# Optimization experiments

Measured on AMD Instinct MI355X. Metric: run time of the kernel, lower is better.

The kernel has to match this reference:

```python
import jax, jax.numpy as jnp
import numpy as np

KS = [3, 3, 7, 7, 11, 11, 21, 21]  # TEXT_KERNEL_SIZES
KMAX = 21
H = 8
D_MODEL = 1024
D_H = D_MODEL // H
R = 4
B = 2
N = 4096


def _extract_windows_1d(xh, k):
    # xh: (B, n, d_h) -> windows: (B, n, k, d_h), zero-padded, stride 1
    pad = k // 2
    xp = jnp.pad(xh, ((0, 0), (pad, pad), (0, 0)))
    idx = jnp.arange(xh.shape[1])[:, None] + jnp.arange(k)[None, :]  # (n, k)
    return xp[:, idx]  # (B, n, k, d_h)


def setup_inputs() -> dict:
    key = jax.random.key(0)
    ks = jax.random.split(key, 10)
    s = 0.02
    return {
        "x": jax.random.normal(ks[0], (B, N, D_MODEL), dtype=jnp.float32),
        "W_in": jax.random.normal(ks[1], (D_MODEL, D_MODEL), dtype=jnp.float32) * s,
        "b_in": jnp.zeros((D_MODEL,), dtype=jnp.float32),
        "W_out": jax.random.normal(ks[2], (D_MODEL, D_MODEL), dtype=jnp.float32) * (0.02 / np.sqrt(2.0 * 8)),
        "b_out": jnp.zeros((D_MODEL,), dtype=jnp.float32),
        "Wc": jax.random.normal(ks[3], (H, D_H, R), dtype=jnp.float32) * s,  # per-token coeff proj
        "A": jax.random.normal(ks[4], (H, R, KMAX), dtype=jnp.float32) * s,  # rank -> kernel-pos factor (padded to KMAX)
        "V": jax.random.normal(ks[5], (H, R, D_H), dtype=jnp.float32) * s,   # rank -> channel factor
        "base": jax.random.normal(ks[6], (H, KMAX, D_H), dtype=jnp.float32) * s,  # static kernel (padded)
        "alphas": jnp.zeros((H,), dtype=jnp.float32),  # sigmoid gate params
    }


def reference(x, W_in, b_in, W_out, b_out, Wc, A, V, base, alphas):
    Bsz, n, d = x.shape
    x_proj = x @ W_in.T + b_in                        # (B, n, d_model)
    x_heads = x_proj.reshape(Bsz, n, H, D_H)          # (B, n, H, d_h)
    head_outs = []
    for h in range(H):
        k = KS[h]
        x_h = x_heads[:, :, h, :]                     # (B, n, d_h)
        # Factored per-token kernel generation
        c = x_h @ Wc[h]                               # (B, n, R)
        dyn = jnp.einsum('bnr,rk,rd->bnkd', c, A[h, :, :k], V[h])  # (B, n, k, d_h)
        alpha = jax.nn.sigmoid(alphas[h])
        K_hat = alpha * dyn + (1.0 - alpha) * base[h, :k][None, None]  # (B, n, k, d_h)
        windows = _extract_windows_1d(x_h, k)         # (B, n, k, d_h)
        o_h = jnp.einsum('bnkd,bnkd->bnd', K_hat, windows)
        head_outs.append(o_h)
    concat = jnp.concatenate(head_outs, axis=-1)      # (B, n, d_model)
    return concat @ W_out.T + b_out
```

## Files before the change

### kernel.cpp

```cpp
#include <hip/hip_runtime.h>
#include <stdint.h>

typedef __bf16 bf16;
typedef __bf16 bf16x8 __attribute__((ext_vector_type(8)));
typedef float f32x4 __attribute__((ext_vector_type(4)));

#define AS1 __attribute__((address_space(1)))
#define AS3 __attribute__((address_space(3)))

__device__ __forceinline__ void gload_lds16(const void* g, void* l) {
    __builtin_amdgcn_global_load_lds((const AS1 uint32_t*)g, (AS3 uint32_t*)l, 16, 0, 0);
}

#define BM 128
#define BN 128
#define BK 32

__global__ __launch_bounds__(256, 2) void gemm_nt(
    const bf16* __restrict__ A, const bf16* __restrict__ B,
    const float* __restrict__ bias, float* __restrict__ C,
    int M, int N, int K)
{
    __shared__ bf16 smA[BM * BK];
    __shared__ bf16 smB[BN * BK];

    const int tid  = threadIdx.x;
    const int wave = tid >> 6;
    const int lane = tid & 63;
    const int wm = (wave >> 1) * 64;
    const int wn = (wave & 1) * 64;
    const int rowA0 = blockIdx.x * BM;
    const int rowB0 = blockIdx.y * BN;

    f32x4 acc[4][4] = {};

    const int g  = lane >> 4;
    const int rm = lane & 15;

    for (int k0 = 0; k0 < K; k0 += BK) {
        #pragma unroll
        for (int i = 0; i < 2; ++i) {
            int slot = i * 256 + tid;
            int row  = slot >> 2;
            int kgs  = slot & 3;
            int kd   = kgs ^ ((row >> 1) & 3);
            const bf16* ga = A + (size_t)(rowA0 + row) * K + k0 + kd * 8;
            const bf16* gb = B + (size_t)(rowB0 + row) * K + k0 + kd * 8;
            int ldsbase = (i * 256 + (wave << 6)) * 8;
            gload_lds16(ga, &smA[ldsbase]);
            gload_lds16(gb, &smB[ldsbase]);
        }
        __syncthreads();

        bf16x8 af[4], bfr[4];
        #pragma unroll
        for (int mi = 0; mi < 4; ++mi) {
            int row  = wm + mi * 16 + rm;
            int slot = row * 4 + (g ^ ((row >> 1) & 3));
            af[mi] = *(const bf16x8*)&smA[slot * 8];
        }
        #pragma unroll
        for (int ni = 0; ni < 4; ++ni) {
            int row  = wn + ni * 16 + rm;
            int slot = row * 4 + (g ^ ((row >> 1) & 3));
            bfr[ni] = *(const bf16x8*)&smB[slot * 8];
        }
        #pragma unroll
        for (int mi = 0; mi < 4; ++mi)
            #pragma unroll
            for (int ni = 0; ni < 4; ++ni)
                acc[mi][ni] = __builtin_amdgcn_mfma_f32_16x16x32_bf16(
                    af[mi], bfr[ni], acc[mi][ni], 0, 0, 0);
        __syncthreads();
    }

    const int quad = lane >> 4;
    #pragma unroll
    for (int ni = 0; ni < 4; ++ni) {
        int col = rowB0 + wn + ni * 16 + rm;
        float bcol = bias[col];
        #pragma unroll
        for (int mi = 0; mi < 4; ++mi) {
            #pragma unroll
            for (int r = 0; r < 4; ++r) {
                int rowc = rowA0 + wm + mi * 16 + quad * 4 + r;
                C[(size_t)rowc * N + col] = acc[mi][ni][r] + bcol;
            }
        }
    }
}

__global__ void cast_all_kernel(const float* __restrict__ x, bf16* __restrict__ xb,
                                const float* __restrict__ wi, bf16* __restrict__ wib,
                                const float* __restrict__ wo, bf16* __restrict__ wob)
{
    const int NX8 = (2 * 4096 * 1024) / 8;
    const int NW8 = (1024 * 1024) / 8;
    int i = blockIdx.x * 256 + threadIdx.x;
    const float* in; bf16* out; int idx;
    if (i < NX8)            { in = x;  out = xb;  idx = i; }
    else if (i < NX8 + NW8) { in = wi; out = wib; idx = i - NX8; }
    else                    { in = wo; out = wob; idx = i - NX8 - NW8; }
    const float4* p = (const float4*)in;
    float4 a = p[2 * idx], b = p[2 * idx + 1];
    bf16x8 o;
    o[0] = (bf16)a.x; o[1] = (bf16)a.y; o[2] = (bf16)a.z; o[3] = (bf16)a.w;
    o[4] = (bf16)b.x; o[5] = (bf16)b.y; o[6] = (bf16)b.z; o[7] = (bf16)b.w;
    *(bf16x8*)(out + 8 * idx) = o;
}

__global__ __launch_bounds__(256) void c_compute(
    const float* __restrict__ xp, const float* __restrict__ Wc,
    float* __restrict__ cbuf)
{
    const int wave = threadIdx.x >> 6, lane = threadIdx.x & 63;
    const int row  = blockIdx.x * 4 + wave;
    const int h    = lane >> 3;
    const int d0   = (lane & 7) * 16;

    const float4* xr = (const float4*)(xp + (size_t)row * 1024 + lane * 16);
    float p0 = 0.f, p1 = 0.f, p2 = 0.f, p3 = 0.f;
    #pragma unroll
    for (int q = 0; q < 4; ++q) {
        float4 xv = xr[q];
        float vals[4] = {xv.x, xv.y, xv.z, xv.w};
        #pragma unroll
        for (int i = 0; i < 4; ++i) {
            float4 wr = *(const float4*)(Wc + h * 512 + (d0 + q * 4 + i) * 4);
            float x = vals[i];
            p0 += x * wr.x; p1 += x * wr.y; p2 += x * wr.z; p3 += x * wr.w;
        }
    }
    #pragma unroll
    for (int off = 1; off <= 4; off <<= 1) {
        p0 += __shfl_xor(p0, off);
        p1 += __shfl_xor(p1, off);
        p2 += __shfl_xor(p2, off);
        p3 += __shfl_xor(p3, off);
    }
    if ((lane & 7) == 0) {
        float4 o = {p0, p1, p2, p3};
        *(float4*)(cbuf + (size_t)row * 32 + h * 4) = o;
    }
}

__constant__ int KS_c[8] = {3, 3, 7, 7, 11, 11, 21, 21};

template <int K>
__device__ __forceinline__ void mix_body(
    int h, int d, int n0, const float* __restrict__ xp,
    const float* __restrict__ cbuf, const float* __restrict__ Aw,
    const float* __restrict__ Vw, const float* __restrict__ basew,
    float alpha, bf16* __restrict__ y)
{
    constexpr int T = 8;
    constexpr int W = T + K - 1;
    constexpr int pad = K / 2;
    const int nloc = n0 & 4095;

    float w[W];
    #pragma unroll
    for (int j = 0; j < W; ++j) {
        int nl = nloc + j - pad;
        bool valid = (nl >= 0) && (nl < 4096);
        w[j] = valid ? xp[(size_t)(n0 + j - pad) * 1024 + h * 128 + d] : 0.f;
    }

    float s0[T] = {}, s1[T] = {}, s2[T] = {}, s3[T] = {}, tv[T] = {};
    const float* Ah = Aw + h * 84;
    const float* bh = basew + h * 2688 + d;
    #pragma unroll
    for (int j = 0; j < K; ++j) {
        float a0 = Ah[j], a1 = Ah[21 + j], a2 = Ah[42 + j], a3 = Ah[63 + j];
        float bbj = bh[j * 128];
        #pragma unroll
        for (int t = 0; t < T; ++t) {
            float x = w[t + j];
            s0[t] += a0 * x; s1[t] += a1 * x;
            s2[t] += a2 * x; s3[t] += a3 * x;
            tv[t] += bbj * x;
        }
    }

    float v0 = Vw[h * 512 + d],       v1 = Vw[h * 512 + 128 + d];
    float v2 = Vw[h * 512 + 256 + d], v3 = Vw[h * 512 + 384 + d];
    #pragma unroll
    for (int t = 0; t < T; ++t) {
        float4 c4 = *(const float4*)(cbuf + (size_t)(n0 + t) * 32 + h * 4);
        float o = alpha * (c4.x * v0 * s0[t] + c4.y * v1 * s1[t] +
                           c4.z * v2 * s2[t] + c4.w * v3 * s3[t])
                + (1.f - alpha) * tv[t];
        y[(size_t)(n0 + t) * 1024 + h * 128 + d] = (bf16)o;
    }
}

__global__ __launch_bounds__(256) void head_mix2(
    const float* __restrict__ xp, const float* __restrict__ cbuf,
    const float* __restrict__ Aw, const float* __restrict__ Vw,
    const float* __restrict__ basew, const float* __restrict__ alphas,
    bf16* __restrict__ y)
{
    const int h   = blockIdx.x;
    const int d   = threadIdx.x & 127;
    const int sub = threadIdx.x >> 7;
    const int n0  = (blockIdx.y * 2 + sub) * 8;
    const float alpha = 1.f / (1.f + __expf(-alphas[h]));

    switch (KS_c[h]) {
        case 3:  mix_body<3>(h, d, n0, xp, cbuf, Aw, Vw, basew, alpha, y); break;
        case 7:  mix_body<7 >(h, d, n0, xp, cbuf, Aw, Vw, basew, alpha, y); break;
        case 11: mix_body<11>(h, d, n0, xp, cbuf, Aw, Vw, basew, alpha, y); break;
        default: mix_body<21>(h, d, n0, xp, cbuf, Aw, Vw, basew, alpha, y); break;
    }
}

extern "C" void kernel_launch(void* const* d_in, const int* in_sizes, int n_in,
                              void* d_out, int out_size, void* d_ws, size_t ws_size,
                              hipStream_t stream)
{
    const float* x      = (const float*)d_in[0];
    const float* W_in   = (const float*)d_in[1];
    const float* b_in   = (const float*)d_in[2];
    const float* W_out  = (const float*)d_in[3];
    const float* b_out  = (const float*)d_in[4];
    const float* Wc     = (const float*)d_in[5];
    const float* Aw     = (const float*)d_in[6];
    const float* Vw     = (const float*)d_in[7];
    const float* basew  = (const float*)d_in[8];
    const float* alphas = (const float*)d_in[9];
    float* out = (float*)d_out;

    const size_t MB = 1u << 20;
    char* ws = (char*)d_ws;
    bf16*  xb   = (bf16*) (ws);
    bf16*  wib  = (bf16*) (ws + 16 * MB);
    bf16*  wob  = (bf16*) (ws + 18 * MB);
    float* xp   = (float*)(ws + 20 * MB);
    bf16*  yb   = (bf16*) (ws + 52 * MB);
    float* cbuf = (float*)(ws + 68 * MB);

    const int NTOT8 = (2 * 4096 * 1024 + 2 * 1024 * 1024) / 8;

    cast_all_kernel<<<NTOT8 / 256, 256, 0, stream>>>(x, xb, W_in, wib, W_out, wob);

    gemm_nt<<<dim3(8192 / BM, 1024 / BN), 256, 0, stream>>>(
        xb, wib, b_in, xp, 8192, 1024, 1024);

    c_compute<<<8192 / 4, 256, 0, stream>>>(xp, Wc, cbuf);

    head_mix2<<<dim3(8, 512), 256, 0, stream>>>(
        xp, cbuf, Aw, Vw, basew, alphas, yb);

    gemm_nt<<<dim3(8192 / BM, 1024 / BN), 256, 0, stream>>>(
        yb, wob, b_out, out, 8192, 1024, 1024);
}
```

Measured before the change: 200.7 us.

## Store projected activations in bf16 and double GEMM K-tile to 64

The input projection GEMM now writes its output in bf16 rather than fp32, and the coefficient and head-mix kernels read that bf16 buffer. This halves intermediate write and read traffic. The GEMM K tile also grows from 32 to 64 with a widened XOR swizzle, so each barrier pair now covers two MFMA sub-steps, at the cost of more LDS per block. Precision of the intermediate projection drops to bf16.

Measured after the change: 207.3 us. 1.03x slower.

```diff
diff --git a/kernel.cpp b/kernel.cpp
--- a/kernel.cpp
+++ b/kernel.cpp
@@ -14,11 +14,12 @@
 
 #define BM 128
 #define BN 128
-#define BK 32
-
+#define BK 64
+
+template <typename OT>
 __global__ __launch_bounds__(256, 2) void gemm_nt(
     const bf16* __restrict__ A, const bf16* __restrict__ B,
-    const float* __restrict__ bias, float* __restrict__ C,
+    const float* __restrict__ bias, OT* __restrict__ C,
     int M, int N, int K)
 {
     __shared__ bf16 smA[BM * BK];
@@ -39,11 +40,11 @@
 
     for (int k0 = 0; k0 < K; k0 += BK) {
         #pragma unroll
-        for (int i = 0; i < 2; ++i) {
+        for (int i = 0; i < 4; ++i) {
             int slot = i * 256 + tid;
-            int row  = slot >> 2;
-            int kgs  = slot & 3;
-            int kd   = kgs ^ ((row >> 1) & 3);
+            int row  = slot >> 3;
+            int kgs  = slot & 7;
+            int kd   = kgs ^ ((row >> 1) & 7);
             const bf16* ga = A + (size_t)(rowA0 + row) * K + k0 + kd * 8;
             const bf16* gb = B + (size_t)(rowB0 + row) * K + k0 + kd * 8;
             int ldsbase = (i * 256 + (wave << 6)) * 8;
@@ -52,25 +53,28 @@
         }
         __syncthreads();
 
-        bf16x8 af[4], bfr[4];
-        #pragma unroll
-        for (int mi = 0; mi < 4; ++mi) {
-            int row  = wm + mi * 16 + rm;
-            int slot = row * 4 + (g ^ ((row >> 1) & 3));
-            af[mi] = *(const bf16x8*)&smA[slot * 8];
-        }
-        #pragma unroll
-        for (int ni = 0; ni < 4; ++ni) {
-            int row  = wn + ni * 16 + rm;
-            int slot = row * 4 + (g ^ ((row >> 1) & 3));
-            bfr[ni] = *(const bf16x8*)&smB[slot * 8];
-        }
-        #pragma unroll
-        for (int mi = 0; mi < 4; ++mi)
-            #pragma unroll
-            for (int ni = 0; ni < 4; ++ni)
-                acc[mi][ni] = __builtin_amdgcn_mfma_f32_16x16x32_bf16(
-                    af[mi], bfr[ni], acc[mi][ni], 0, 0, 0);
+        #pragma unroll
+        for (int s = 0; s < 2; ++s) {
+            bf16x8 af[4], bfr[4];
+            #pragma unroll
+            for (int mi = 0; mi < 4; ++mi) {
+                int row  = wm + mi * 16 + rm;
+                int slot = row * 8 + ((s * 4 + g) ^ ((row >> 1) & 7));
+                af[mi] = *(const bf16x8*)&smA[slot * 8];
+            }
+            #pragma unroll
+            for (int ni = 0; ni < 4; ++ni) {
+                int row  = wn + ni * 16 + rm;
+                int slot = row * 8 + ((s * 4 + g) ^ ((row >> 1) & 7));
+                bfr[ni] = *(const bf16x8*)&smB[slot * 8];
+            }
+            #pragma unroll
+            for (int mi = 0; mi < 4; ++mi)
+                #pragma unroll
+                for (int ni = 0; ni < 4; ++ni)
+                    acc[mi][ni] = __builtin_amdgcn_mfma_f32_16x16x32_bf16(
+                        af[mi], bfr[ni], acc[mi][ni], 0, 0, 0);
+        }
         __syncthreads();
     }
 
@@ -84,7 +88,7 @@
             #pragma unroll
             for (int r = 0; r < 4; ++r) {
                 int rowc = rowA0 + wm + mi * 16 + quad * 4 + r;
-                C[(size_t)rowc * N + col] = acc[mi][ni][r] + bcol;
+                C[(size_t)rowc * N + col] = (OT)(acc[mi][ni][r] + bcol);
             }
         }
     }
@@ -110,7 +114,7 @@
 }
 
 __global__ __launch_bounds__(256) void c_compute(
-    const float* __restrict__ xp, const float* __restrict__ Wc,
+    const bf16* __restrict__ xpb, const float* __restrict__ Wc,
     float* __restrict__ cbuf)
 {
     const int wave = threadIdx.x >> 6, lane = threadIdx.x & 63;
@@ -118,18 +122,15 @@
     const int h    = lane >> 3;
     const int d0   = (lane & 7) * 16;
 
-    const float4* xr = (const float4*)(xp + (size_t)row * 1024 + lane * 16);
+    const bf16* xr = xpb + (size_t)row * 1024 + lane * 16;
+    bf16x8 v0 = *(const bf16x8*)xr;
+    bf16x8 v1 = *(const bf16x8*)(xr + 8);
     float p0 = 0.f, p1 = 0.f, p2 = 0.f, p3 = 0.f;
     #pragma unroll
-    for (int q = 0; q < 4; ++q) {
-        float4 xv = xr[q];
-        float vals[4] = {xv.x, xv.y, xv.z, xv.w};
-        #pragma unroll
-        for (int i = 0; i < 4; ++i) {
-            float4 wr = *(const float4*)(Wc + h * 512 + (d0 + q * 4 + i) * 4);
-            float x = vals[i];
-            p0 += x * wr.x; p1 += x * wr.y; p2 += x * wr.z; p3 += x * wr.w;
-        }
+    for (int i = 0; i < 16; ++i) {
+        float xv = (i < 8) ? (float)v0[i & 7] : (float)v1[i & 7];
+        float4 wr = *(const float4*)(Wc + h * 512 + (d0 + i) * 4);
+        p0 += xv * wr.x; p1 += xv * wr.y; p2 += xv * wr.z; p3 += xv * wr.w;
     }
     #pragma unroll
     for (int off = 1; off <= 4; off <<= 1) {
@@ -148,7 +149,7 @@
 
 template <int K>
 __device__ __forceinline__ void mix_body(
-    int h, int d, int n0, const float* __restrict__ xp,
+    int h, int d, int n0, const bf16* __restrict__ xpb,
     const float* __restrict__ cbuf, const float* __restrict__ Aw,
     const float* __restrict__ Vw, const float* __restrict__ basew,
     float alpha, bf16* __restrict__ y)
@@ -163,7 +164,7 @@
     for (int j = 0; j < W; ++j) {
         int nl = nloc + j - pad;
         bool valid = (nl >= 0) && (nl < 4096);
-        w[j] = valid ? xp[(size_t)(n0 + j - pad) * 1024 + h * 128 + d] : 0.f;
+        w[j] = valid ? (float)xpb[(size_t)(n0 + j - pad) * 1024 + h * 128 + d] : 0.f;
     }
 
     float s0[T] = {}, s1[T] = {}, s2[T] = {}, s3[T] = {}, tv[T] = {};
@@ -195,7 +196,7 @@
 }
 
 __global__ __launch_bounds__(256) void head_mix2(
-    const float* __restrict__ xp, const float* __restrict__ cbuf,
+    const bf16* __restrict__ xpb, const float* __restrict__ cbuf,
     const float* __restrict__ Aw, const float* __restrict__ Vw,
     const float* __restrict__ basew, const float* __restrict__ alphas,
     bf16* __restrict__ y)
@@ -207,10 +208,10 @@
     const float alpha = 1.f / (1.f + __expf(-alphas[h]));
 
     switch (KS_c[h]) {
-        case 3:  mix_body<3>(h, d, n0, xp, cbuf, Aw, Vw, basew, alpha, y); break;
-        case 7:  mix_body<7 >(h, d, n0, xp, cbuf, Aw, Vw, basew, alpha, y); break;
-        case 11: mix_body<11>(h, d, n0, xp, cbuf, Aw, Vw, basew, alpha, y); break;
-        default: mix_body<21>(h, d, n0, xp, cbuf, Aw, Vw, basew, alpha, y); break;
+        case 3:  mix_body<3>(h, d, n0, xpb, cbuf, Aw, Vw, basew, alpha, y); break;
+        case 7:  mix_body<7 >(h, d, n0, xpb, cbuf, Aw, Vw, basew, alpha, y); break;
+        case 11: mix_body<11>(h, d, n0, xpb, cbuf, Aw, Vw, basew, alpha, y); break;
+        default: mix_body<21>(h, d, n0, xpb, cbuf, Aw, Vw, basew, alpha, y); break;
     }
 }
 
@@ -235,22 +236,22 @@
     bf16*  xb   = (bf16*) (ws);
     bf16*  wib  = (bf16*) (ws + 16 * MB);
     bf16*  wob  = (bf16*) (ws + 18 * MB);
-    float* xp   = (float*)(ws + 20 * MB);
-    bf16*  yb   = (bf16*) (ws + 52 * MB);
-    float* cbuf = (float*)(ws + 68 * MB);
+    bf16*  xpb  = (bf16*) (ws + 20 * MB);
+    bf16*  yb   = (bf16*) (ws + 36 * MB);
+    float* cbuf = (float*)(ws + 52 * MB);
 
     const int NTOT8 = (2 * 4096 * 1024 + 2 * 1024 * 1024) / 8;
 
     cast_all_kernel<<<NTOT8 / 256, 256, 0, stream>>>(x, xb, W_in, wib, W_out, wob);
 
-    gemm_nt<<<dim3(8192 / BM, 1024 / BN), 256, 0, stream>>>(
-        xb, wib, b_in, xp, 8192, 1024, 1024);
-
-    c_compute<<<8192 / 4, 256, 0, stream>>>(xp, Wc, cbuf);
+    gemm_nt<bf16><<<dim3(8192 / BM, 1024 / BN), 256, 0, stream>>>(
+        xb, wib, b_in, xpb, 8192, 1024, 1024);
+
+    c_compute<<<8192 / 4, 256, 0, stream>>>(xpb, Wc, cbuf);
 
     head_mix2<<<dim3(8, 512), 256, 0, stream>>>(
-        xp, cbuf, Aw, Vw, basew, alphas, yb);
-
-    gemm_nt<<<dim3(8192 / BM, 1024 / BN), 256, 0, stream>>>(
+        xpb, cbuf, Aw, Vw, basew, alphas, yb);
+
+    gemm_nt<float><<<dim3(8192 / BM, 1024 / BN), 256, 0, stream>>>(
         yb, wob, b_out, out, 8192, 1024, 1024);
 }
```
